# Kernel optimization log

Measured on AMD Instinct MI355X. Metric: run time of the kernel, lower is better.

Reference implementation:

```python
import jax, jax.numpy as jnp
import numpy as np

K, D, P, C = 96, 256, 40, 8  # trials, embed dim, phoneme bins, gate hidden

def setup_inputs() -> dict:
    key = jax.random.key(0)
    ks = jax.random.split(key, 5)
    return {
        "enroll": jax.random.normal(ks[0], (K, D, P), jnp.float32),
        "test": jax.random.normal(ks[1], (K, D, P), jnp.float32),
        "fc1_w": jax.random.normal(ks[2], (C, 1), jnp.float32) * 0.5,
        "fc1_b": jax.random.normal(ks[3], (C,), jnp.float32) * 0.1,
        "fc2_w": jax.random.normal(ks[4], (1, C), jnp.float32) * 0.5,
    }

def _l2norm(x, axis):
    # torch F.normalize(p=2): x / max(||x||, eps)
    n = jnp.sqrt(jnp.sum(x * x, axis=axis, keepdims=True))
    return x / jnp.maximum(n, 1e-12)

def _gate(x, fc1_w, fc1_b, fc2_w):
    # tiny 1->C->1 MLP: fc2(tanh(fc1(x))), applied elementwise on x
    h = jnp.tanh(x[..., None] * fc1_w[:, 0] + fc1_b)   # [..., C]
    return jnp.einsum('...c,c->...', h, fc2_w[0])

def reference(enroll, test, fc1_w, fc1_b, fc2_w):
    e = _l2norm(enroll, axis=1)                        # [K, D, P]
    t = _l2norm(test, axis=1)                          # [K, D, P]
    # pho_matrix[k,l,i,j] = <e[k,:,i], t[l,:,j]>
    pho = jnp.einsum('kdi,ldj->klij', e, t)            # [K, K, P, P]
    cnt1 = jnp.sum(pho != 0, axis=-1).astype(pho.dtype) + 1e-6
    pho = _gate(pho, fc1_w, fc1_b, fc2_w) * pho        # gated elementwise
    pho = jnp.sum(pho, axis=-1) / cnt1                 # [K, K, P]
    cnt2 = jnp.sum(pho != 0, axis=-1).astype(pho.dtype) + 1e-6
    pho = _gate(pho, fc1_w, fc1_b, fc2_w) * pho        # [K, K, P]
    return jnp.sum(pho, axis=-1) / cnt2                # [K, K]
```

## Files before the change

kernel.cpp:

```cpp
#include <hip/hip_runtime.h>
#include <math.h>

#define KTR 96
#define DIM 256
#define PB  40
#define CH  8
#define MDIM 3840
#define KK  512
#define BM 160
#define BN 128
#define BK 32
#define LDA 40
#define NTAB 2113
#define TPAD 2120

typedef _Float16 v8h __attribute__((ext_vector_type(8)));
typedef float    v4f __attribute__((ext_vector_type(4)));

__device__ __forceinline__ float gate_ref(float x, const float* w, const float* b, const float* v) {
    float g = 0.f;
    #pragma unroll
    for (int c = 0; c < CH; ++c) g = fmaf(v[c], tanhf(fmaf(w[c], x, b[c])), g);
    return g;
}

__global__ __launch_bounds__(256) void k_norm(const float* __restrict__ enroll,
                                              const float* __restrict__ test,
                                              const float* __restrict__ fc1_w,
                                              const float* __restrict__ fc1_b,
                                              const float* __restrict__ fc2_w,
                                              _Float16* __restrict__ XT,
                                              _Float16* __restrict__ XE,
                                              float2* __restrict__ gtabG) {
    int b = blockIdx.x, tid = threadIdx.x;

    if (b >= 2 * KTR) {
        int i = (b - 2 * KTR) * 256 + tid;
        if (i < NTAB) {
            float w[CH], bb[CH], vv[CH];
            #pragma unroll
            for (int c = 0; c < CH; ++c) { w[c] = fc1_w[c]; bb[c] = fc1_b[c]; vv[c] = fc2_w[c]; }
            float g0 = gate_ref((float)(i - 1056) * 0.0009765625f, w, bb, vv);
            float g1 = gate_ref((float)(i - 1055) * 0.0009765625f, w, bb, vv);
            gtabG[i] = make_float2(g0, g1 - g0);
        }
        return;
    }

    bool isE = (b < KTR);
    int k = isE ? b : b - KTR;
    const float* src = (isE ? enroll : test) + (size_t)k * DIM * PB;

    __shared__ float S[DIM * 41];
    __shared__ float part[6 * PB];
    __shared__ float rn[PB];

    for (int i = tid; i < DIM * PB / 4; i += 256) {
        float4 v = ((const float4*)src)[i];
        int d = i / 10, c = i - d * 10;
        float* p = &S[d * 41 + c * 4];
        p[0] = v.x; p[1] = v.y; p[2] = v.z; p[3] = v.w;
    }
    __syncthreads();
    if (tid < 240) {
        int g = tid / PB, p = tid - (tid / PB) * PB;
        float acc = 0.f;
        for (int d = g; d < DIM; d += 6) {
            float x = S[d * 41 + p];
            acc = fmaf(x, x, acc);
        }
        part[g * PB + p] = acc;
    }
    __syncthreads();
    if (tid < PB) {
        float s = 0.f;
        #pragma unroll
        for (int g = 0; g < 6; ++g) s += part[g * PB + tid];
        rn[tid] = 1.0f / fmaxf(sqrtf(s), 1e-12f);
    }
    __syncthreads();

    int d = tid;
    for (int p = 0; p < PB; ++p) {
        float v = S[d * 41 + p] * rn[p];
        _Float16 h  = (_Float16)v;
        _Float16 lo = (_Float16)((v - (float)h) * 4096.0f);
        size_t m = (size_t)(k * PB + p);
        if (isE) { XE[m * KK + d] = lo; XE[m * KK + 256 + d] = h;  }
        else     { XT[m * KK + d] = h;  XT[m * KK + 256 + d] = lo; }
    }
}

__global__ __launch_bounds__(256, 3) void k_gemm(const _Float16* __restrict__ XT,
                                                 const _Float16* __restrict__ XE,
                                                 const float2* __restrict__ gtabG,
                                                 float* __restrict__ pho2) {
    __shared__ __align__(16) _Float16 LA[BM * LDA];
    __shared__ __align__(16) _Float16 LB[BN * LDA];
    __shared__ float gval[TPAD];
    __shared__ float gslope[TPAD];

    int tid  = threadIdx.x;
    int lane = tid & 63;
    int wv   = tid >> 6;

    for (int i = tid; i < NTAB; i += 256) {
        float2 t = gtabG[i];
        gval[i] = t.x; gslope[i] = t.y;
    }

    int m0 = blockIdx.y * BM;
    int n0 = blockIdx.x * BN;
    int wm = (wv & 1) * 80;
    int wn = (wv >> 1) * 64;
    int r15 = lane & 15;
    int q4  = lane >> 4;

    v4f acc[5][4];
    #pragma unroll
    for (int mt = 0; mt < 5; ++mt)
        #pragma unroll
        for (int nt = 0; nt < 4; ++nt)
            acc[mt][nt] = (v4f)0.f;

    int aoff[5], boff[4];
    #pragma unroll
    for (int mt = 0; mt < 5; ++mt) aoff[mt] = (wm + mt * 16 + r15) * LDA + q4 * 8;
    #pragma unroll
    for (int nt = 0; nt < 4; ++nt) boff[nt] = (wn + nt * 16 + r15) * LDA + q4 * 8;

    int arow = tid >> 2, aqc = tid & 3;
    const uint4* gT = (const uint4*)(XT + (size_t)(m0 + arow) * KK);
    const uint4* gE = (const uint4*)(XE + (size_t)(n0 + arow) * KK);
    uint4* lA = (uint4*)LA + (arow * 5 + aqc);
    uint4* lB = (uint4*)LB + (arow * 5 + aqc);

    uint4 va0, va1, va2, vb0, vb1;
    #define LOADS(IT) {                                                     \
        int ka = ((IT) < 16) ? (IT) * BK : ((IT) - 16) * BK;                \
        int kb = ((IT) < 16) ? (IT) * BK : 256 + ((IT) - 16) * BK;          \
        int ia = (ka >> 3) + aqc, ib = (kb >> 3) + aqc;                     \
        va0 = gT[ia]; va1 = gT[ia + 64 * 64];                               \
        if (tid < 128) va2 = gT[ia + 128 * 64];                             \
        vb0 = gE[ib]; vb1 = gE[ib + 64 * 64]; }

    LOADS(0);
    for (int it = 0; it < 24; ++it) {
        __syncthreads();
        lA[0]   = va0;
        lA[320] = va1;
        if (tid < 128) lA[640] = va2;
        lB[0]   = vb0;
        lB[320] = vb1;
        __syncthreads();

        if (it < 23) LOADS(it + 1);

        if (it == 16) {
            #pragma unroll
            for (int mt = 0; mt < 5; ++mt)
                #pragma unroll
                for (int nt = 0; nt < 4; ++nt)
                    acc[mt][nt] *= 0.000244140625f;
        }

        v8h af[5], bf[4];
        #pragma unroll
        for (int mt = 0; mt < 5; ++mt) af[mt] = *(const v8h*)(LA + aoff[mt]);
        #pragma unroll
        for (int nt = 0; nt < 4; ++nt) bf[nt] = *(const v8h*)(LB + boff[nt]);
        #pragma unroll
        for (int mt = 0; mt < 5; ++mt)
            #pragma unroll
            for (int nt = 0; nt < 4; ++nt)
                acc[mt][nt] = __builtin_amdgcn_mfma_f32_16x16x32_f16(af[mt], bf[nt], acc[mt][nt], 0, 0, 0);
    }
    #undef LOADS

    const float inv40 = 1.0f / (40.0f + 1e-6f);
    int lg = (m0 + wm) / PB;
    #pragma unroll
    for (int nt = 0; nt < 4; ++nt) {
        float s0 = 0.f, s1 = 0.f, t2 = 0.f;
        #pragma unroll
        for (int mt = 0; mt < 5; ++mt) {
            #pragma unroll
            for (int r = 0; r < 4; ++r) {
                float x = acc[mt][nt][r];
                float u = fmaf(x, 1024.0f, 1056.0f);
                int i = (int)u;
                i = min(max(i, 0), NTAB - 2);
                float f = u - (float)i;
                float g = fmaf(f, gslope[i], gval[i]);
                float xg = g * x;
                if (mt < 2)       s0 += xg;
                else if (mt == 2) t2 += xg;
                else              s1 += xg;
            }
        }
        bool lo = (q4 < 2);
        s0 += lo ? t2 : 0.f;
        s1 += lo ? 0.f : t2;
        s0 += __shfl_xor(s0, 16); s0 += __shfl_xor(s0, 32);
        s1 += __shfl_xor(s1, 16); s1 += __shfl_xor(s1, 32);
        if (q4 == 0) {
            int n = n0 + wn + nt * 16 + r15;
            int kk = n / PB, ii = n - kk * PB;
            pho2[((size_t)kk * KTR + lg)     * PB + ii] = s0 * inv40;
            pho2[((size_t)kk * KTR + lg + 1) * PB + ii] = s1 * inv40;
        }
    }
}

__global__ __launch_bounds__(256) void k_final(const float* __restrict__ pho2,
                                               const float* __restrict__ fc1_w,
                                               const float* __restrict__ fc1_b,
                                               const float* __restrict__ fc2_w,
                                               float* __restrict__ out) {
    int wv = threadIdx.x >> 6;
    int lane = threadIdx.x & 63;
    int pair = blockIdx.x * 4 + wv;

    float w[CH], bb[CH], vv[CH];
    #pragma unroll
    for (int c = 0; c < CH; ++c) { w[c] = fc1_w[c]; bb[c] = fc1_b[c]; vv[c] = fc2_w[c]; }

    float x = (lane < PB) ? pho2[(size_t)pair * PB + lane] : 0.f;
    float s = gate_ref(x, w, bb, vv) * x;

    #pragma unroll
    for (int off = 32; off; off >>= 1) s += __shfl_xor(s, off);
    if (lane == 0) out[pair] = s / (40.0f + 1e-6f);
}

extern "C" void kernel_launch(void* const* d_in, const int* in_sizes, int n_in,
                              void* d_out, int out_size, void* d_ws, size_t ws_size,
                              hipStream_t stream) {
    const float* enroll = (const float*)d_in[0];
    const float* test   = (const float*)d_in[1];
    const float* fc1_w  = (const float*)d_in[2];
    const float* fc1_b  = (const float*)d_in[3];
    const float* fc2_w  = (const float*)d_in[4];
    float* out = (float*)d_out;

    _Float16* XT = (_Float16*)d_ws;
    _Float16* XE = XT + (size_t)MDIM * KK;
    float* pho2  = (float*)(XE + (size_t)MDIM * KK);
    float2* gtabG = (float2*)(pho2 + (size_t)KTR * KTR * PB);

    k_norm<<<2 * KTR + 9, 256, 0, stream>>>(enroll, test, fc1_w, fc1_b, fc2_w, XT, XE, gtabG);
    dim3 g2(MDIM / BN, MDIM / BM);
    k_gemm<<<g2, 256, 0, stream>>>(XT, XE, gtabG, pho2);
    k_final<<<KTR * KTR / 4, 256, 0, stream>>>(pho2, fc1_w, fc1_b, fc2_w, out);
}
```

Before: 111.0 us.

## Stream GEMM tiles directly into swizzled double-buffered LDS via global_load_lds

Operand tiles in the GEMM kernel no longer pass through registers. Each thread now issues 16-byte global_load_lds copies straight into LDS, into one of two buffers in turn, and the padded layout is replaced by an XOR-swizzled one to avoid bank conflicts. This cuts the VGPR staging, the explicit LDS stores and one barrier per iteration, so the next tile's load overlaps the MFMAs on the current tile. In exchange LDS use per block grows, which puts pressure on the three-blocks-per-CU occupancy target. Correctness depends on the barrier waiting for the async loads to finish.

```diff
diff --git a/kernel.cpp b/kernel.cpp
--- a/kernel.cpp
+++ b/kernel.cpp
@@ -10,7 +10,6 @@
 #define BM 160
 #define BN 128
 #define BK 32
-#define LDA 40
 #define NTAB 2113
 #define TPAD 2120
 
@@ -22,6 +21,11 @@
     #pragma unroll
     for (int c = 0; c < CH; ++c) g = fmaf(v[c], tanhf(fmaf(w[c], x, b[c])), g);
     return g;
+}
+
+__device__ __forceinline__ void gload16(const _Float16* g, _Float16* l) {
+    __builtin_amdgcn_global_load_lds((const __attribute__((address_space(1))) void*)g,
+                                     (__attribute__((address_space(3))) void*)l, 16, 0, 0);
 }
 
 __global__ __launch_bounds__(256) void k_norm(const float* __restrict__ enroll,
@@ -95,8 +99,8 @@
                                                  const _Float16* __restrict__ XE,
                                                  const float2* __restrict__ gtabG,
                                                  float* __restrict__ pho2) {
-    __shared__ __align__(16) _Float16 LA[BM * LDA];
-    __shared__ __align__(16) _Float16 LB[BN * LDA];
+    __shared__ __align__(16) _Float16 LA[2][BM * BK];
+    __shared__ __align__(16) _Float16 LB[2][BN * BK];
     __shared__ float gval[TPAD];
     __shared__ float gslope[TPAD];
 
@@ -123,38 +127,48 @@
         for (int nt = 0; nt < 4; ++nt)
             acc[mt][nt] = (v4f)0.f;
 
+    int cs = ((q4 ^ ((r15 >> 1) & 3)) << 3);
     int aoff[5], boff[4];
     #pragma unroll
-    for (int mt = 0; mt < 5; ++mt) aoff[mt] = (wm + mt * 16 + r15) * LDA + q4 * 8;
-    #pragma unroll
-    for (int nt = 0; nt < 4; ++nt) boff[nt] = (wn + nt * 16 + r15) * LDA + q4 * 8;
-
-    int arow = tid >> 2, aqc = tid & 3;
-    const uint4* gT = (const uint4*)(XT + (size_t)(m0 + arow) * KK);
-    const uint4* gE = (const uint4*)(XE + (size_t)(n0 + arow) * KK);
-    uint4* lA = (uint4*)LA + (arow * 5 + aqc);
-    uint4* lB = (uint4*)LB + (arow * 5 + aqc);
-
-    uint4 va0, va1, va2, vb0, vb1;
-    #define LOADS(IT) {                                                     \
-        int ka = ((IT) < 16) ? (IT) * BK : ((IT) - 16) * BK;                \
-        int kb = ((IT) < 16) ? (IT) * BK : 256 + ((IT) - 16) * BK;          \
-        int ia = (ka >> 3) + aqc, ib = (kb >> 3) + aqc;                     \
-        va0 = gT[ia]; va1 = gT[ia + 64 * 64];                               \
-        if (tid < 128) va2 = gT[ia + 128 * 64];                             \
-        vb0 = gE[ib]; vb1 = gE[ib + 64 * 64]; }
-
-    LOADS(0);
+    for (int mt = 0; mt < 5; ++mt) aoff[mt] = (wm + mt * 16 + r15) * BK + cs;
+    #pragma unroll
+    for (int nt = 0; nt < 4; ++nt) boff[nt] = (wn + nt * 16 + r15) * BK + cs;
+
+    int ag[3], bg[2];
+    #pragma unroll
+    for (int i = 0; i < 3; ++i) {
+        int cid = i * 256 + tid;
+        int r = cid >> 2;
+        int q = (cid & 3) ^ ((r >> 1) & 3);
+        ag[i] = (m0 + r) * KK + q * 8;
+    }
+    #pragma unroll
+    for (int i = 0; i < 2; ++i) {
+        int cid = i * 256 + tid;
+        int r = cid >> 2;
+        int q = (cid & 3) ^ ((r >> 1) & 3);
+        bg[i] = (n0 + r) * KK + q * 8;
+    }
+
+    #define STAGE(c, ka, kb) {                                              \
+        const _Float16* gA = XT + (ka);                                     \
+        const _Float16* gB = XE + (kb);                                     \
+        gload16(gA + ag[0], &LA[c][0 * 2048 + wv * 512]);                   \
+        gload16(gA + ag[1], &LA[c][1 * 2048 + wv * 512]);                   \
+        if (tid < 128) gload16(gA + ag[2], &LA[c][2 * 2048 + wv * 512]);    \
+        gload16(gB + bg[0], &LB[c][0 * 2048 + wv * 512]);                   \
+        gload16(gB + bg[1], &LB[c][1 * 2048 + wv * 512]); }
+
+    STAGE(0, 0, 0)
+    int cur = 0;
     for (int it = 0; it < 24; ++it) {
         __syncthreads();
-        lA[0]   = va0;
-        lA[320] = va1;
-        if (tid < 128) lA[640] = va2;
-        lB[0]   = vb0;
-        lB[320] = vb1;
-        __syncthreads();
-
-        if (it < 23) LOADS(it + 1);
+        if (it < 23) {
+            int nx = it + 1;
+            int ka = (nx < 16) ? nx * BK : (nx - 16) * BK;
+            int kb = (nx < 16) ? nx * BK : 256 + (nx - 16) * BK;
+            STAGE(cur ^ 1, ka, kb)
+        }
 
         if (it == 16) {
             #pragma unroll
@@ -164,18 +178,22 @@
                     acc[mt][nt] *= 0.000244140625f;
         }
 
+        const _Float16* la = LA[cur];
+        const _Float16* lb = LB[cur];
         v8h af[5], bf[4];
         #pragma unroll
-        for (int mt = 0; mt < 5; ++mt) af[mt] = *(const v8h*)(LA + aoff[mt]);
-        #pragma unroll
-        for (int nt = 0; nt < 4; ++nt) bf[nt] = *(const v8h*)(LB + boff[nt]);
+        for (int mt = 0; mt < 5; ++mt) af[mt] = *(const v8h*)(la + aoff[mt]);
+        #pragma unroll
+        for (int nt = 0; nt < 4; ++nt) bf[nt] = *(const v8h*)(lb + boff[nt]);
         #pragma unroll
         for (int mt = 0; mt < 5; ++mt)
             #pragma unroll
             for (int nt = 0; nt < 4; ++nt)
                 acc[mt][nt] = __builtin_amdgcn_mfma_f32_16x16x32_f16(af[mt], bf[nt], acc[mt][nt], 0, 0, 0);
-    }
-    #undef LOADS
+
+        cur ^= 1;
+    }
+    #undef STAGE
 
     const float inv40 = 1.0f / (40.0f + 1e-6f);
     int lg = (m0 + wm) / PB;
```

Measured after the change: 120.8 us. +8.8%, slower.

## Load B fragments directly from global into registers and swizzle block order

Applied to the files above, without the earlier changes.

The B operand (enroll rows) no longer goes through LDS. Each wave now loads its MFMA B fragments straight from global memory into double-buffered registers, and the K loop is fully unrolled. Workgroup IDs are remapped so that blocks which share rows are scheduled together, which should improve L2 reuse. Launch bounds drop from 3 to 2 blocks per SIMD to make room for the extra registers, which lowers occupancy, and each wave issues redundant global loads for B that were previously shared through LDS.

```diff
diff --git a/kernel.cpp b/kernel.cpp
--- a/kernel.cpp
+++ b/kernel.cpp
@@ -91,12 +91,11 @@
     }
 }
 
-__global__ __launch_bounds__(256, 3) void k_gemm(const _Float16* __restrict__ XT,
+__global__ __launch_bounds__(256, 2) void k_gemm(const _Float16* __restrict__ XT,
                                                  const _Float16* __restrict__ XE,
                                                  const float2* __restrict__ gtabG,
                                                  float* __restrict__ pho2) {
     __shared__ __align__(16) _Float16 LA[BM * LDA];
-    __shared__ __align__(16) _Float16 LB[BN * LDA];
     __shared__ float gval[TPAD];
     __shared__ float gslope[TPAD];
 
@@ -109,8 +108,10 @@
         gval[i] = t.x; gslope[i] = t.y;
     }
 
-    int m0 = blockIdx.y * BM;
-    int n0 = blockIdx.x * BN;
+    int id = blockIdx.y * 30 + blockIdx.x;
+    int wg = (id & 7) * 90 + (id >> 3);
+    int m0 = (wg / 30) * BM;
+    int n0 = (wg % 30) * BN;
     int wm = (wv & 1) * 80;
     int wn = (wv >> 1) * 64;
     int r15 = lane & 15;
@@ -123,38 +124,49 @@
         for (int nt = 0; nt < 4; ++nt)
             acc[mt][nt] = (v4f)0.f;
 
-    int aoff[5], boff[4];
+    int aoff[5];
     #pragma unroll
     for (int mt = 0; mt < 5; ++mt) aoff[mt] = (wm + mt * 16 + r15) * LDA + q4 * 8;
-    #pragma unroll
-    for (int nt = 0; nt < 4; ++nt) boff[nt] = (wn + nt * 16 + r15) * LDA + q4 * 8;
+
+    const _Float16* pb[4];
+    #pragma unroll
+    for (int nt = 0; nt < 4; ++nt) pb[nt] = XE + (size_t)(n0 + wn + nt * 16 + r15) * KK + q4 * 8;
 
     int arow = tid >> 2, aqc = tid & 3;
     const uint4* gT = (const uint4*)(XT + (size_t)(m0 + arow) * KK);
-    const uint4* gE = (const uint4*)(XE + (size_t)(n0 + arow) * KK);
     uint4* lA = (uint4*)LA + (arow * 5 + aqc);
-    uint4* lB = (uint4*)LB + (arow * 5 + aqc);
-
-    uint4 va0, va1, va2, vb0, vb1;
-    #define LOADS(IT) {                                                     \
+
+    uint4 va0, va1, va2;
+    #define LOADSA(IT) {                                                    \
         int ka = ((IT) < 16) ? (IT) * BK : ((IT) - 16) * BK;                \
+        int ia = (ka >> 3) + aqc;                                           \
+        va0 = gT[ia]; va1 = gT[ia + 64 * 64];                               \
+        if (tid < 128) va2 = gT[ia + 128 * 64]; }
+
+    v8h B0[4], B1[4];
+    #define GLDB(Sb, IT) {                                                  \
         int kb = ((IT) < 16) ? (IT) * BK : 256 + ((IT) - 16) * BK;          \
-        int ia = (ka >> 3) + aqc, ib = (kb >> 3) + aqc;                     \
-        va0 = gT[ia]; va1 = gT[ia + 64 * 64];                               \
-        if (tid < 128) va2 = gT[ia + 128 * 64];                             \
-        vb0 = gE[ib]; vb1 = gE[ib + 64 * 64]; }
-
-    LOADS(0);
+        _Pragma("unroll") for (int nt = 0; nt < 4; ++nt) Sb[nt] = *(const v8h*)(pb[nt] + kb); }
+
+    #define MFMAS(AF, BF) {                                                 \
+        _Pragma("unroll") for (int mt = 0; mt < 5; ++mt)                    \
+        _Pragma("unroll") for (int nt = 0; nt < 4; ++nt)                    \
+            acc[mt][nt] = __builtin_amdgcn_mfma_f32_16x16x32_f16(AF[mt], BF[nt], acc[mt][nt], 0, 0, 0); }
+
+    LOADSA(0);
+    GLDB(B0, 0);
+    #pragma unroll
     for (int it = 0; it < 24; ++it) {
         __syncthreads();
         lA[0]   = va0;
         lA[320] = va1;
         if (tid < 128) lA[640] = va2;
-        lB[0]   = vb0;
-        lB[320] = vb1;
         __syncthreads();
 
-        if (it < 23) LOADS(it + 1);
+        if (it < 23) {
+            LOADSA(it + 1);
+            if (it & 1) { GLDB(B0, it + 1) } else { GLDB(B1, it + 1) }
+        }
 
         if (it == 16) {
             #pragma unroll
@@ -164,18 +176,14 @@
                     acc[mt][nt] *= 0.000244140625f;
         }
 
-        v8h af[5], bf[4];
+        v8h af[5];
         #pragma unroll
         for (int mt = 0; mt < 5; ++mt) af[mt] = *(const v8h*)(LA + aoff[mt]);
-        #pragma unroll
-        for (int nt = 0; nt < 4; ++nt) bf[nt] = *(const v8h*)(LB + boff[nt]);
-        #pragma unroll
-        for (int mt = 0; mt < 5; ++mt)
-            #pragma unroll
-            for (int nt = 0; nt < 4; ++nt)
-                acc[mt][nt] = __builtin_amdgcn_mfma_f32_16x16x32_f16(af[mt], bf[nt], acc[mt][nt], 0, 0, 0);
-    }
-    #undef LOADS
+        if (it & 1) { MFMAS(af, B1) } else { MFMAS(af, B0) }
+    }
+    #undef LOADSA
+    #undef GLDB
+    #undef MFMAS
 
     const float inv40 = 1.0f / (40.0f + 1e-6f);
     int lg = (m0 + wm) / PB;
```

Result: slower. 161.7 us (+45.7%).
